# Kernel optimization log

Measured on AMD Instinct MI355X. Metric: run time of the kernel, lower is better.

The kernel has to match this reference:

```python
import jax, jax.numpy as jnp
import numpy as np

B, S, D, H = 4, 2048, 768, 12


def setup_inputs() -> dict:
    key = jax.random.key(0)
    k1, k2, k3, k4 = jax.random.split(key, 4)
    std = D ** (-0.5)
    x = jax.random.normal(k1, (B, S, D), dtype=jnp.float32)
    W_QKV = jax.random.normal(k2, (3, D, D), dtype=jnp.float32) * std
    W_O = jax.random.normal(k3, (D, D), dtype=jnp.float32) * std
    token_positions = jnp.sort(jax.random.randint(k4, (B, S), 0, S), axis=-1).astype(jnp.int64)
    return {"x": x, "W_QKV": W_QKV, "W_O": W_O, "token_positions": token_positions,
            "num_heads": H, "theta": 10000}


def _apply_rope(t, cos, sin):
    # t: (B, H, S, Hd); cos/sin: (B, 1, S, Hd/2). Interleaved even/odd pairs.
    te, to = t[..., 0::2], t[..., 1::2]
    re = te * cos - to * sin
    ro = te * sin + to * cos
    return jnp.stack([re, ro], axis=-1).reshape(t.shape)


def reference(x, W_QKV, W_O, token_positions, num_heads, theta):
    b, s, d = x.shape
    hd = d // num_heads  # d_head = d_k = d_v
    # fused QKV projection: Q = x @ W_QKV[0].T etc.
    qkv = jnp.einsum('bsd,kod->kbso', x, W_QKV)              # (3, B, S, D)
    qkv = qkv.reshape(3, b, s, num_heads, hd).transpose(0, 1, 3, 2, 4)  # (3, B, H, S, Hd)
    q, k, v = qkv[0], qkv[1], qkv[2]
    # RoPE angles: pos * theta^(-2j/d_k)
    inv_freq = jnp.asarray(theta, x.dtype) ** (-(jnp.arange(0, hd, 2, dtype=x.dtype) / hd))
    angles = token_positions.astype(x.dtype)[..., None] * inv_freq    # (B, S, Hd/2)
    cos = jnp.cos(angles)[:, None]                                     # (B, 1, S, Hd/2)
    sin = jnp.sin(angles)[:, None]
    q = _apply_rope(q, cos, sin)
    k = _apply_rope(k, cos, sin)
    # causal attention
    scores = jnp.einsum('bhqd,bhkd->bhqk', q, k) / (hd ** 0.5)        # (B, H, S, S)
    causal = jnp.tril(jnp.ones((s, s), dtype=bool))
    scores = jnp.where(causal, scores, -jnp.inf)
    probs = jax.nn.softmax(scores, axis=-1)
    out = jnp.einsum('bhqk,bhkd->bhqd', probs, v)                      # (B, H, S, Hd)
    out = out.transpose(0, 2, 1, 3).reshape(b, s, d)
    return out @ W_O.T
```

## Files before the change

### kernel.cpp

```cpp
#include <hip/hip_runtime.h>
#include <hip/hip_bf16.h>

typedef __bf16 bf16;
typedef __bf16 bf16x8 __attribute__((ext_vector_type(8)));
typedef __bf16 bf16x4 __attribute__((ext_vector_type(4)));
typedef short  s16x4  __attribute__((ext_vector_type(4)));
typedef float  f32x4  __attribute__((ext_vector_type(4)));

#if defined(__has_builtin)
#if __has_builtin(__builtin_amdgcn_mfma_f32_16x16x16bf16_1k)
#define HAVE_MFMA16 1
#endif
#if __has_builtin(__builtin_amdgcn_exp2f)
#define EXP2(x) __builtin_amdgcn_exp2f(x)
#else
#define EXP2(x) exp2f(x)
#endif
#else
#define EXP2(x) exp2f(x)
#endif

__device__ __forceinline__ void gl_lds16(const void* g, void* l) {
  __builtin_amdgcn_global_load_lds(
      (__attribute__((address_space(1))) const void*)g,
      (__attribute__((address_space(3))) void*)l, 16, 0, 0);
}

__device__ __forceinline__ f32x4 mfma32(bf16x8 a, bf16x8 b, f32x4 c) {
  return __builtin_amdgcn_mfma_f32_16x16x32_bf16(a, b, c, 0, 0, 0);
}
#if HAVE_MFMA16
__device__ __forceinline__ f32x4 mfma16(s16x4 a, s16x4 b, f32x4 c) {
  return __builtin_amdgcn_mfma_f32_16x16x16bf16_1k(a, b, c, 0, 0, 0);
}
#endif

__global__ void prep(const float* __restrict__ a, bf16* __restrict__ da,
                     const float* __restrict__ b, bf16* __restrict__ db,
                     const float* __restrict__ c, bf16* __restrict__ dc,
                     const int* __restrict__ tpos, const int* __restrict__ thetap,
                     float2* __restrict__ tab) {
  int bx = blockIdx.x;
  if (bx >= 8448) {
    int i = (bx - 8448) * 256 + threadIdx.x;
    int d2 = i & 31;
    int bs = i >> 5;
    float lt = log2f((float)(*thetap));
    float fr = exp2f(-(float)d2 * (1.0f / 32.0f) * lt);
    float ang = (float)tpos[bs] * fr;
    float sn, cs;
    sincosf(ang, &sn, &cs);
    tab[i] = make_float2(cs, sn);
    return;
  }
  const float* s; bf16* d; int i;
  if (bx < 6144)      { s = a; d = da; i = bx * 256 + threadIdx.x; }
  else if (bx < 7872) { s = b; d = db; i = (bx - 6144) * 256 + threadIdx.x; }
  else                { s = c; d = dc; i = (bx - 7872) * 256 + threadIdx.x; }
  float4 v = ((const float4*)s)[i];
  bf16x4 o;
  o[0] = (bf16)v.x; o[1] = (bf16)v.y; o[2] = (bf16)v.z; o[3] = (bf16)v.w;
  ((bf16x4*)d)[i] = o;
}

__global__ void gemm_qkv(const bf16* __restrict__ A, const bf16* __restrict__ Bm,
                         bf16* __restrict__ Cout, bf16* __restrict__ Vout,
                         const float2* __restrict__ tab) {
  constexpr int K = 768;
  __shared__ __align__(16) char As[2][128 * 64];
  __shared__ __align__(16) char Bs[2][128 * 64];
  const int tid = threadIdx.x;
  const int w = tid >> 6, lane = tid & 63;
  const int quad = lane >> 4, l15 = lane & 15;
  const int wrow = w >> 1, wcol = w & 1;
  const int m0 = blockIdx.x * 128, n0 = blockIdx.y * 128;

  f32x4 acc[4][4];
#pragma unroll
  for (int mt = 0; mt < 4; ++mt)
#pragma unroll
    for (int nt = 0; nt < 4; ++nt) acc[mt][nt] = (f32x4){0.f, 0.f, 0.f, 0.f};

  auto stage = [&](int k0, int bufi) {
#pragma unroll
    for (int i = 0; i < 2; ++i) {
      int L = i * 256 + tid;
      int r = L >> 2, cl = L & 3;
      int cg = cl ^ ((r >> 1) & 3);
      gl_lds16(A + (size_t)(m0 + r) * K + k0 + cg * 8, As[bufi] + (i * 256 + w * 64) * 16);
      gl_lds16(Bm + (size_t)(n0 + r) * K + k0 + cg * 8, Bs[bufi] + (i * 256 + w * 64) * 16);
    }
  };

  stage(0, 0);
  int buf = 0;

  for (int k0 = 0; k0 < K; k0 += 32) {
    __syncthreads();
    if (k0 + 32 < K) stage(k0 + 32, buf ^ 1);
    const char* Ab = As[buf];
    const char* Bb = Bs[buf];

    bf16x8 af[4], bfr[4];
#pragma unroll
    for (int mt = 0; mt < 4; ++mt) {
      int r = wrow * 64 + mt * 16 + l15;
      int cl = quad ^ ((r >> 1) & 3);
      af[mt] = *(const bf16x8*)(Ab + r * 64 + cl * 16);
    }
#pragma unroll
    for (int nt = 0; nt < 4; ++nt) {
      int r = wcol * 64 + nt * 16 + l15;
      int cl = quad ^ ((r >> 1) & 3);
      bfr[nt] = *(const bf16x8*)(Bb + r * 64 + cl * 16);
    }
#pragma unroll
    for (int mt = 0; mt < 4; ++mt)
#pragma unroll
      for (int nt = 0; nt < 4; ++nt)
        acc[mt][nt] = mfma32(af[mt], bfr[nt], acc[mt][nt]);
    buf ^= 1;
  }

#pragma unroll
  for (int mt = 0; mt < 4; ++mt)
#pragma unroll
    for (int nt = 0; nt < 4; ++nt)
#pragma unroll
      for (int r = 0; r < 4; ++r) {
        int m = m0 + wrow * 64 + mt * 16 + quad * 4 + r;
        int n = n0 + wcol * 64 + nt * 16 + l15;
        float v = acc[mt][nt][r];
        int mat = n / 768, rem = n % 768;
        int hh = rem >> 6, d = rem & 63;
        int bb = m >> 11, s = m & 2047;
        if (mat == 2) {
          Vout[(((size_t)(bb * 12 + hh) * 64 + d) * 2048) + s] = (bf16)v;
        } else {
          float partner = __shfl_xor(v, 1);
          float2 t = tab[((size_t)m << 5) + ((rem >> 1) & 31)];
          float out = v * t.x + ((n & 1) ? partner : -partner) * t.y;
          if (mat == 0) out *= 0.18033688011112042f;
          Cout[(((size_t)(mat * 4 + bb) * 12 + hh) * 2048 + s) * 64 + d] = (bf16)out;
        }
      }
}

__global__ __launch_bounds__(256, 4)
void gemm_o(const bf16* __restrict__ A, const bf16* __restrict__ Bm,
            float* __restrict__ Cout) {
  constexpr int K = 768;
  __shared__ __align__(16) char As[2][64 * 64];
  __shared__ __align__(16) char Bs[2][128 * 64];
  const int tid = threadIdx.x;
  const int w = tid >> 6, lane = tid & 63;
  const int quad = lane >> 4, l15 = lane & 15;
  const int wrow = w >> 1, wcol = w & 1;
  const int f = blockIdx.x;
  const int xcd = f & 7, j = f >> 3;
  const int m0 = (xcd * 16 + j / 6) * 64;
  const int n0 = (j % 6) * 128;

  f32x4 acc[2][4];
#pragma unroll
  for (int mt = 0; mt < 2; ++mt)
#pragma unroll
    for (int nt = 0; nt < 4; ++nt) acc[mt][nt] = (f32x4){0.f, 0.f, 0.f, 0.f};

  auto stage = [&](int k0, int bufi) {
    {
      int L = tid;
      int r = L >> 2, cl = L & 3;
      int cg = cl ^ ((r >> 1) & 3);
      gl_lds16(A + (size_t)(m0 + r) * K + k0 + cg * 8, As[bufi] + (w * 64) * 16 + lane * 16);
    }
#pragma unroll
    for (int i = 0; i < 2; ++i) {
      int L = i * 256 + tid;
      int r = L >> 2, cl = L & 3;
      int cg = cl ^ ((r >> 1) & 3);
      gl_lds16(Bm + (size_t)(n0 + r) * K + k0 + cg * 8, Bs[bufi] + (i * 256 + w * 64) * 16);
    }
  };

  stage(0, 0);
  int buf = 0;

  for (int k0 = 0; k0 < K; k0 += 32) {
    __syncthreads();
    if (k0 + 32 < K) stage(k0 + 32, buf ^ 1);
    const char* Ab = As[buf];
    const char* Bb = Bs[buf];

    bf16x8 af[2], bfr[4];
#pragma unroll
    for (int mt = 0; mt < 2; ++mt) {
      int r = wrow * 32 + mt * 16 + l15;
      int cl = quad ^ ((r >> 1) & 3);
      af[mt] = *(const bf16x8*)(Ab + r * 64 + cl * 16);
    }
#pragma unroll
    for (int nt = 0; nt < 4; ++nt) {
      int r = wcol * 64 + nt * 16 + l15;
      int cl = quad ^ ((r >> 1) & 3);
      bfr[nt] = *(const bf16x8*)(Bb + r * 64 + cl * 16);
    }
#pragma unroll
    for (int mt = 0; mt < 2; ++mt)
#pragma unroll
      for (int nt = 0; nt < 4; ++nt)
        acc[mt][nt] = mfma32(af[mt], bfr[nt], acc[mt][nt]);
    buf ^= 1;
  }

#pragma unroll
  for (int mt = 0; mt < 2; ++mt)
#pragma unroll
    for (int nt = 0; nt < 4; ++nt)
#pragma unroll
      for (int r = 0; r < 4; ++r) {
        int m = m0 + wrow * 32 + mt * 16 + quad * 4 + r;
        int n = n0 + wcol * 64 + nt * 16 + l15;
        Cout[(size_t)m * 768 + n] = acc[mt][nt][r];
      }
}

__global__ __launch_bounds__(128, 3)
void attn(const bf16* __restrict__ qkv, const bf16* __restrict__ vt,
          bf16* __restrict__ aout) {
  const int bx = blockIdx.x;
  const int xcd = bx & 7, jb = bx >> 3;
  const int qt = 31 - (jb / 6);
  const int bh = xcd * 6 + (jb % 6);
  const int b = bh / 12, h = bh % 12;
  const int tid = threadIdx.x, w = tid >> 6, lane = tid & 63;
  const int quad = lane >> 4, l15 = lane & 15;
  const bf16* Q  = qkv + (size_t)bh * (2048 * 64);
  const bf16* Kp = qkv + (size_t)(48 + bh) * (2048 * 64);
  const bf16* Vt = vt + (size_t)bh * (64 * 2048);
  __shared__ __align__(16) char Ks[2][64 * 128];
  __shared__ __align__(16) char Vs[2][64 * 128];

  const int qbase = qt * 64 + w * 32;
  bf16x8 qf[2][2];
#pragma unroll
  for (int j = 0; j < 2; ++j) {
    qf[j][0] = *(const bf16x8*)(Q + (size_t)(qbase + j * 16 + l15) * 64 + quad * 8);
    qf[j][1] = *(const bf16x8*)(Q + (size_t)(qbase + j * 16 + l15) * 64 + 32 + quad * 8);
  }

  float li[2] = {0.f, 0.f};
  f32x4 o[2][4];
#pragma unroll
  for (int j = 0; j < 2; ++j)
#pragma unroll
    for (int dt = 0; dt < 4; ++dt) o[j][dt] = (f32x4){0.f, 0.f, 0.f, 0.f};

  auto stage = [&](int kb, int bufi) {
#pragma unroll
    for (int i = 0; i < 4; ++i) {
      int L = i * 128 + tid;
      int r = L >> 3, cl = L & 7, cg = cl ^ (r & 7);
      gl_lds16(Kp + (size_t)(kb * 64 + r) * 64 + cg * 8, Ks[bufi] + L * 16);
      gl_lds16(Vt + (size_t)r * 2048 + kb * 64 + cg * 8, Vs[bufi] + L * 16);
    }
  };

  stage(0, 0);
  int buf = 0;

  for (int kb = 0; kb <= qt; ++kb) {
    __syncthreads();
    if (kb < qt) stage(kb + 1, buf ^ 1);
    const char* Kb = Ks[buf];
    const char* Vb = Vs[buf];

    float S[2][16];
#pragma unroll
    for (int sk = 0; sk < 4; ++sk) {
      int r = sk * 16 + l15;
      int cl0 = quad ^ (r & 7);
      int cl1 = (4 + quad) ^ (r & 7);
      bf16x8 kf0 = *(const bf16x8*)(Kb + r * 128 + cl0 * 16);
      bf16x8 kf1 = *(const bf16x8*)(Kb + r * 128 + cl1 * 16);
#pragma unroll
      for (int j = 0; j < 2; ++j) {
        f32x4 st = (f32x4){0.f, 0.f, 0.f, 0.f};
        st = mfma32(kf0, qf[j][0], st);
        st = mfma32(kf1, qf[j][1], st);
#pragma unroll
        for (int rr = 0; rr < 4; ++rr) S[j][sk * 4 + rr] = st[rr];
      }
    }
    if (kb == qt) {
#pragma unroll
      for (int j = 0; j < 2; ++j)
#pragma unroll
        for (int sk = 0; sk < 4; ++sk)
#pragma unroll
          for (int rr = 0; rr < 4; ++rr) {
            int key = kb * 64 + sk * 16 + quad * 4 + rr;
            if (key > qbase + j * 16 + l15) S[j][sk * 4 + rr] = -1e30f;
          }
    }

#if HAVE_MFMA16
    s16x4 pf[2][4];
#endif
#pragma unroll
    for (int j = 0; j < 2; ++j) {
      float rs = 0.f;
#pragma unroll
      for (int sk = 0; sk < 4; ++sk) {
        bf16x4 pb;
#pragma unroll
        for (int rr = 0; rr < 4; ++rr) {
          float p = EXP2(S[j][sk * 4 + rr]);
          rs += p;
          pb[rr] = (bf16)p;
#if !HAVE_MFMA16
          S[j][sk * 4 + rr] = p;
#endif
        }
#if HAVE_MFMA16
        pf[j][sk] = __builtin_bit_cast(s16x4, pb);
#else
        (void)pb;
#endif
      }
      rs += __shfl_xor(rs, 16);
      rs += __shfl_xor(rs, 32);
      li[j] += rs;
    }

#if HAVE_MFMA16
#pragma unroll
    for (int sk = 0; sk < 4; ++sk)
#pragma unroll
      for (int dt = 0; dt < 4; ++dt) {
        int rr = dt * 16 + l15;
        int c = sk * 2 + (quad >> 1);
        int cl = c ^ (rr & 7);
        s16x4 vf = *(const s16x4*)(Vb + rr * 128 + cl * 16 + (quad & 1) * 8);
        o[0][dt] = mfma16(pf[0][sk], vf, o[0][dt]);
        o[1][dt] = mfma16(pf[1][sk], vf, o[1][dt]);
      }
#else
#pragma unroll
    for (int j = 0; j < 2; ++j)
#pragma unroll
      for (int kc = 0; kc < 2; ++kc) {
        bf16x8 af;
#pragma unroll
        for (int jj = 0; jj < 8; ++jj) {
          int sq = (quad & 1) * 2 + (jj >> 2);
          int src = sq * 16 + l15;
          float v0 = __shfl(S[j][kc * 8 + (jj & 3)], src);
          float v1 = __shfl(S[j][kc * 8 + 4 + (jj & 3)], src);
          af[jj] = (bf16)((quad < 2) ? v0 : v1);
        }
#pragma unroll
        for (int dt = 0; dt < 4; ++dt) {
          int rr = dt * 16 + l15;
          int c = kc * 4 + quad;
          int cl = c ^ (rr & 7);
          bf16x8 vf = *(const bf16x8*)(Vb + rr * 128 + cl * 16);
          o[j][dt] = mfma32(af, vf, o[j][dt]);
        }
      }
#endif
    buf ^= 1;
  }

#pragma unroll
  for (int j = 0; j < 2; ++j) {
    float lr[4];
#pragma unroll
    for (int rr = 0; rr < 4; ++rr)
      lr[rr] = __builtin_amdgcn_rcpf(__shfl(li[j], quad * 4 + rr));
#pragma unroll
    for (int dt = 0; dt < 4; ++dt)
#pragma unroll
      for (int rr = 0; rr < 4; ++rr) {
        int q = qbase + j * 16 + quad * 4 + rr;
        int n = h * 64 + dt * 16 + l15;
        aout[((size_t)b * 2048 + q) * 768 + n] = (bf16)(o[j][dt][rr] * lr[rr]);
      }
  }
}

extern "C" void kernel_launch(void* const* d_in, const int* in_sizes, int n_in,
                              void* d_out, int out_size, void* d_ws, size_t ws_size,
                              hipStream_t stream) {
  const float* x    = (const float*)d_in[0];
  const float* wqkv = (const float*)d_in[1];
  const float* wo   = (const float*)d_in[2];
  const int* tpos   = (const int*)d_in[3];
  const int* thetap = (const int*)d_in[5];

  char* ws = (char*)d_ws;
  bf16* xb    = (bf16*)(ws);
  bf16* wqkvb = (bf16*)(ws + 12582912);
  bf16* wob   = (bf16*)(ws + 16121856);
  bf16* qkv   = (bf16*)(ws + 17301504);
  bf16* vtb   = (bf16*)(ws + 55050240);
  float2* tab = (float2*)(ws + 42467328);

  prep<<<9472, 256, 0, stream>>>(x, xb, wqkv, wqkvb, wo, wob, tpos, thetap, tab);
  gemm_qkv<<<dim3(64, 18), 256, 0, stream>>>(xb, wqkvb, qkv, vtb, tab);
  attn<<<1536, 128, 0, stream>>>(qkv, vtb, xb);
  gemm_o<<<768, 256, 0, stream>>>(xb, wob, (float*)d_out);
}
```

Baseline: 220.0 us.

## Stage V transpose through LDS for coalesced stores; add launch bounds and MFMA priority

The QKV GEMM epilogue for the V matrix now transposes each tile through shared memory, reusing the merged A/B staging buffer, and writes contiguous 16-byte chunks along the sequence dimension. This replaces the old strided scalar bf16 stores. The GEMM also gets launch_bounds(256,4) to target higher occupancy. The attention kernel raises wave priority around its MFMA blocks with s_setprio so matrix work is issued ahead of other waves. The trade-offs are extra LDS round trips and barriers in the epilogue, plus possible register pressure from the launch bound.

```diff
diff --git a/kernel.cpp b/kernel.cpp
--- a/kernel.cpp
+++ b/kernel.cpp
@@ -63,12 +63,12 @@
   ((bf16x4*)d)[i] = o;
 }
 
-__global__ void gemm_qkv(const bf16* __restrict__ A, const bf16* __restrict__ Bm,
-                         bf16* __restrict__ Cout, bf16* __restrict__ Vout,
-                         const float2* __restrict__ tab) {
+__global__ __launch_bounds__(256, 4)
+void gemm_qkv(const bf16* __restrict__ A, const bf16* __restrict__ Bm,
+              bf16* __restrict__ Cout, bf16* __restrict__ Vout,
+              const float2* __restrict__ tab) {
   constexpr int K = 768;
-  __shared__ __align__(16) char As[2][128 * 64];
-  __shared__ __align__(16) char Bs[2][128 * 64];
+  __shared__ __align__(16) char SM[2][16384];
   const int tid = threadIdx.x;
   const int w = tid >> 6, lane = tid & 63;
   const int quad = lane >> 4, l15 = lane & 15;
@@ -87,8 +87,8 @@
       int L = i * 256 + tid;
       int r = L >> 2, cl = L & 3;
       int cg = cl ^ ((r >> 1) & 3);
-      gl_lds16(A + (size_t)(m0 + r) * K + k0 + cg * 8, As[bufi] + (i * 256 + w * 64) * 16);
-      gl_lds16(Bm + (size_t)(n0 + r) * K + k0 + cg * 8, Bs[bufi] + (i * 256 + w * 64) * 16);
+      gl_lds16(A + (size_t)(m0 + r) * K + k0 + cg * 8, SM[bufi] + (i * 256 + w * 64) * 16);
+      gl_lds16(Bm + (size_t)(n0 + r) * K + k0 + cg * 8, SM[bufi] + 8192 + (i * 256 + w * 64) * 16);
     }
   };
 
@@ -98,8 +98,8 @@
   for (int k0 = 0; k0 < K; k0 += 32) {
     __syncthreads();
     if (k0 + 32 < K) stage(k0 + 32, buf ^ 1);
-    const char* Ab = As[buf];
-    const char* Bb = Bs[buf];
+    const char* Ab = SM[buf];
+    const char* Bb = SM[buf] + 8192;
 
     bf16x8 af[4], bfr[4];
 #pragma unroll
@@ -122,28 +122,62 @@
     buf ^= 1;
   }
 
-#pragma unroll
-  for (int mt = 0; mt < 4; ++mt)
-#pragma unroll
-    for (int nt = 0; nt < 4; ++nt)
-#pragma unroll
-      for (int r = 0; r < 4; ++r) {
-        int m = m0 + wrow * 64 + mt * 16 + quad * 4 + r;
-        int n = n0 + wcol * 64 + nt * 16 + l15;
-        float v = acc[mt][nt][r];
-        int mat = n / 768, rem = n % 768;
-        int hh = rem >> 6, d = rem & 63;
-        int bb = m >> 11, s = m & 2047;
-        if (mat == 2) {
-          Vout[(((size_t)(bb * 12 + hh) * 64 + d) * 2048) + s] = (bf16)v;
-        } else {
+  const int mat = n0 / 768;
+  if (mat == 2) {
+    constexpr int PITCH = 136;
+    bf16* T = (bf16*)&SM[0][0];
+    const int bb = m0 >> 11, s0 = m0 & 2047;
+    const int hh0 = (n0 % 768) >> 6;
+#pragma unroll
+    for (int hh = 0; hh < 2; ++hh) {
+      __syncthreads();
+      if (wcol == hh) {
+#pragma unroll
+        for (int mt = 0; mt < 4; ++mt)
+#pragma unroll
+          for (int nt = 0; nt < 4; ++nt)
+#pragma unroll
+            for (int r = 0; r < 4; ++r) {
+              int s_local = wrow * 64 + mt * 16 + quad * 4 + r;
+              int d_local = nt * 16 + l15;
+              T[d_local * PITCH + s_local] = (bf16)acc[mt][nt][r];
+            }
+      }
+      __syncthreads();
+      {
+        int row = tid >> 2, chunk = tid & 3;
+        const bf16* src = T + row * PITCH + chunk * 32;
+        bf16x8 v0 = ((const bf16x8*)src)[0];
+        bf16x8 v1 = ((const bf16x8*)src)[1];
+        bf16x8 v2 = ((const bf16x8*)src)[2];
+        bf16x8 v3 = ((const bf16x8*)src)[3];
+        bf16* dst = Vout + (((size_t)(bb * 12 + hh0 + hh) * 64 + row) * 2048) + s0 + chunk * 32;
+        ((bf16x8*)dst)[0] = v0;
+        ((bf16x8*)dst)[1] = v1;
+        ((bf16x8*)dst)[2] = v2;
+        ((bf16x8*)dst)[3] = v3;
+      }
+    }
+  } else {
+#pragma unroll
+    for (int mt = 0; mt < 4; ++mt)
+#pragma unroll
+      for (int nt = 0; nt < 4; ++nt)
+#pragma unroll
+        for (int r = 0; r < 4; ++r) {
+          int m = m0 + wrow * 64 + mt * 16 + quad * 4 + r;
+          int n = n0 + wcol * 64 + nt * 16 + l15;
+          float v = acc[mt][nt][r];
+          int rem = n % 768;
+          int hh = rem >> 6, d = rem & 63;
+          int bb = m >> 11, s = m & 2047;
           float partner = __shfl_xor(v, 1);
           float2 t = tab[((size_t)m << 5) + ((rem >> 1) & 31)];
           float out = v * t.x + ((n & 1) ? partner : -partner) * t.y;
           if (mat == 0) out *= 0.18033688011112042f;
           Cout[(((size_t)(mat * 4 + bb) * 12 + hh) * 2048 + s) * 64 + d] = (bf16)out;
         }
-      }
+  }
 }
 
 __global__ __launch_bounds__(256, 4)
@@ -276,6 +310,7 @@
     const char* Vb = Vs[buf];
 
     float S[2][16];
+    __builtin_amdgcn_s_setprio(1);
 #pragma unroll
     for (int sk = 0; sk < 4; ++sk) {
       int r = sk * 16 + l15;
@@ -292,6 +327,7 @@
         for (int rr = 0; rr < 4; ++rr) S[j][sk * 4 + rr] = st[rr];
       }
     }
+    __builtin_amdgcn_s_setprio(0);
     if (kb == qt) {
 #pragma unroll
       for (int j = 0; j < 2; ++j)
@@ -334,6 +370,7 @@
     }
 
 #if HAVE_MFMA16
+    __builtin_amdgcn_s_setprio(1);
 #pragma unroll
     for (int sk = 0; sk < 4; ++sk)
 #pragma unroll
@@ -345,6 +382,7 @@
         o[0][dt] = mfma16(pf[0][sk], vf, o[0][dt]);
         o[1][dt] = mfma16(pf[1][sk], vf, o[1][dt]);
       }
+    __builtin_amdgcn_s_setprio(0);
 #else
 #pragma unroll
     for (int j = 0; j < 2; ++j)
```

Result: faster. 208.6 us (-5.2%).
